# Performance work log

Hardware: AMD Instinct MI355X
Metric: run time of the kernel (lower is better)

## Reference

```python
import jax, jax.numpy as jnp
import numpy as np

BN_EPS = 1e-5
NN_EPS = 1e-8


def _three_nn_interp(xyz1, xyz2, points2):
    # xyz1: [B,N,3], xyz2: [B,S,3], points2: [B,S,D]
    # squared pairwise distances [B,N,S]
    d = (jnp.sum(xyz1 ** 2, -1)[:, :, None]
         + jnp.sum(xyz2 ** 2, -1)[:, None, :]
         - 2.0 * jnp.einsum('bnc,bsc->bns', xyz1, xyz2))
    neg_d3, idx = jax.lax.top_k(-d, 3)          # top-3 smallest dists
    d3 = -neg_d3                                # [B,N,3]
    recip = 1.0 / (d3 + NN_EPS)
    weight = recip / jnp.sum(recip, axis=2, keepdims=True)  # [B,N,3]
    gathered = jax.vmap(lambda p, i: p[i])(points2, idx)    # [B,N,3,D]
    return jnp.sum(gathered * weight[..., None], axis=2)    # [B,N,D]


def _conv_bn_relu(x, w, b, gamma, beta):
    # x: [B,C,N]; 1x1 conv == channel GEMM; BN in training mode (batch stats)
    y = jnp.einsum('oc,bcn->bon', w, x) + b[None, :, None]
    mean = jnp.mean(y, axis=(0, 2), keepdims=True)
    var = jnp.mean((y - mean) ** 2, axis=(0, 2), keepdims=True)
    y = (y - mean) * jax.lax.rsqrt(var + BN_EPS)
    y = y * gamma[None, :, None] + beta[None, :, None]
    return jax.nn.relu(y)


def setup_inputs() -> dict:
    key = jax.random.key(0)
    ks = jax.random.split(key, 8)
    B, N, S, D1, D2 = 8, 8192, 2048, 256, 256
    Cin, C0, C1 = D1 + D2, 256, 256
    return {
        'xyz1': jax.random.normal(ks[0], (B, 3, N), jnp.float32),
        'xyz2': jax.random.normal(ks[1], (B, 3, S), jnp.float32),
        'points1': jax.random.normal(ks[2], (B, D1, N), jnp.float32),
        'points2': jax.random.normal(ks[3], (B, D2, S), jnp.float32),
        'w0': jax.random.normal(ks[4], (C0, Cin), jnp.float32) * (1.0 / np.sqrt(Cin)),
        'b0': jnp.zeros((C0,), jnp.float32),
        'gamma0': jnp.ones((C0,), jnp.float32),
        'beta0': jnp.zeros((C0,), jnp.float32),
        'w1': jax.random.normal(ks[5], (C1, C0), jnp.float32) * (1.0 / np.sqrt(C0)),
        'b1': jnp.zeros((C1,), jnp.float32),
        'gamma1': jnp.ones((C1,), jnp.float32),
        'beta1': jnp.zeros((C1,), jnp.float32),
    }


def reference(xyz1, xyz2, points1, points2, w0, b0, gamma0, beta0, w1, b1, gamma1, beta1):
    x1 = jnp.transpose(xyz1, (0, 2, 1))     # [B,N,3]
    x2 = jnp.transpose(xyz2, (0, 2, 1))     # [B,S,3]
    p2 = jnp.transpose(points2, (0, 2, 1))  # [B,S,D2]
    interp = _three_nn_interp(x1, x2, p2)   # [B,N,D2]
    p1 = jnp.transpose(points1, (0, 2, 1))  # [B,N,D1]
    new_points = jnp.transpose(jnp.concatenate([p1, interp], axis=-1), (0, 2, 1))  # [B,Cin,N]
    h = _conv_bn_relu(new_points, w0, b0, gamma0, beta0)
    return _conv_bn_relu(h, w1, b1, gamma1, beta1)
```

## Files before the change

### kernel.cpp

```cpp
#include <hip/hip_runtime.h>
#include <math.h>

#define B 8
#define N 8192
#define S 2048
#define SCH 1024
#define C 256
#define CIN 512
#define CNT (B * N)
#define NSLOT 1024

typedef unsigned long long ull;
typedef __attribute__((ext_vector_type(8))) short bf16x8;
typedef __attribute__((ext_vector_type(4))) float floatx4;
typedef __attribute__((ext_vector_type(8))) unsigned short ushort8v;
typedef __attribute__((ext_vector_type(4))) unsigned short ushort4v;

__device__ inline unsigned short f2bf(float f) {
  unsigned u = __builtin_bit_cast(unsigned, f);
  u += 0x7FFF + ((u >> 16) & 1);
  return (unsigned short)(u >> 16);
}
__device__ inline float bf2f(unsigned short h) {
  unsigned u = ((unsigned)h) << 16;
  return __builtin_bit_cast(float, u);
}

__device__ inline void load_lds16(const void* g, void* l) {
  __builtin_amdgcn_global_load_lds(
      (const __attribute__((address_space(1))) unsigned int*)g,
      (__attribute__((address_space(3))) unsigned int*)l, 16, 0, 0);
}

__device__ inline void ins3u(ull k, ull& k0, ull& k1, ull& k2) {
  if (k < k2) {
    if (k < k1) {
      k2 = k1;
      if (k < k0) { k1 = k0; k0 = k; } else k1 = k;
    } else k2 = k;
  }
}

__device__ inline void insf(float k, float& m0, float& m1, float& m2) {
  float n1 = __builtin_amdgcn_fmed3f(k, m0, m1);
  float n2 = __builtin_amdgcn_fmed3f(k, m1, m2);
  m0 = fminf(k, m0);
  m1 = n1;
  m2 = n2;
}

__device__ inline unsigned sortkey(float f) {
  unsigned u = __float_as_uint(f);
  return u ^ (((unsigned)((int)u >> 31)) | 0x80000000u);
}
__device__ inline float unsortkey(unsigned u) {
  unsigned m = ((int)u < 0) ? 0x80000000u : 0xFFFFFFFFu;
  return __uint_as_float(u ^ m);
}

#define QDECL(q)                                                            \
  float d0_##q = INFINITY, d1_##q = INFINITY, d2_##q = INFINITY;            \
  float qx_##q, qy_##q, qz_##q, q2_##q;

#define QLOAD(q)                                                            \
  {                                                                         \
    float ox = p1[nq + q], oy = p1[N + nq + q], oz = p1[2 * N + nq + q];    \
    q2_##q = ox * ox + oy * oy + oz * oz;                                   \
    qx_##q = -2.0f * ox; qy_##q = -2.0f * oy; qz_##q = -2.0f * oz;          \
  }

#define QINSD(q)                                                            \
  {                                                                         \
    float d = fmaf(qx_##q, pc.x, fmaf(qy_##q, pc.y, fmaf(qz_##q, pc.z, pc.w))); \
    float n1 = __builtin_amdgcn_fmed3f(d, d0_##q, d1_##q);                  \
    float n2 = __builtin_amdgcn_fmed3f(d, d1_##q, d2_##q);                  \
    d0_##q = fminf(d, d0_##q);                                              \
    d1_##q = n1;                                                            \
    d2_##q = n2;                                                            \
  }

__global__ __launch_bounds__(256, 4) void nn3_kernel(const float* __restrict__ xyz1,
                                                     const float* __restrict__ xyz2,
                                                     const unsigned short* __restrict__ p2t,
                                                     unsigned short* __restrict__ Xb) {
  __shared__ float4 sp[SCH];
  __shared__ float t2q[32];
  __shared__ int ccnt[32];
  __shared__ float cand_d[32][8];
  __shared__ int cand_s[32][8];
  __shared__ int sidx[32][3];
  __shared__ float swt[32][3];
  int b = blockIdx.x >> 8;
  int n0 = (blockIdx.x & 255) * 32;
  const float* p2 = xyz2 + (size_t)b * 3 * S;
  int tid = threadIdx.x;
  int sub = tid & 15, grp = tid >> 4;
  const float* p1 = xyz1 + (size_t)b * 3 * N;
  int nq = n0 + grp * 2;
  QDECL(0) QDECL(1)
  QLOAD(0) QLOAD(1)

  for (int ch = 0; ch < 2; ++ch) {
    if (ch) __syncthreads();
    for (int i = tid; i < SCH; i += 256) {
      int g = ch * SCH + i;
      float px = p2[g], py = p2[S + g], pz = p2[2 * S + g];
      sp[i] = make_float4(px, py, pz, px * px + py * py + pz * pz);
    }
    __syncthreads();
    const float4* spp = sp + sub;
    float4 pc = spp[0];
    for (int t = 0; t < SCH / 16 - 1; ++t) {
      float4 pn = spp[(t + 1) * 16];
      QINSD(0) QINSD(1)
      pc = pn;
    }
    QINSD(0) QINSD(1)
  }

  __syncthreads();
  float* tm = (float*)sp;
  tm[((grp * 2 + 0) * 16 + sub) * 3 + 0] = d0_0;
  tm[((grp * 2 + 0) * 16 + sub) * 3 + 1] = d1_0;
  tm[((grp * 2 + 0) * 16 + sub) * 3 + 2] = d2_0;
  tm[((grp * 2 + 1) * 16 + sub) * 3 + 0] = d0_1;
  tm[((grp * 2 + 1) * 16 + sub) * 3 + 1] = d1_1;
  tm[((grp * 2 + 1) * 16 + sub) * 3 + 2] = d2_1;
  if (tid < 32) ccnt[tid] = 0;
  __syncthreads();
  if (sub < 4) {
#pragma unroll
    for (int q = 0; q < 2; ++q) {
      int qi = grp * 2 + q;
      float m0 = INFINITY, m1 = INFINITY, m2 = INFINITY;
#pragma unroll
      for (int jj = 0; jj < 4; ++jj) {
        int ss = sub + 4 * jj;
        insf(tm[(qi * 16 + ss) * 3 + 0], m0, m1, m2);
        insf(tm[(qi * 16 + ss) * 3 + 1], m0, m1, m2);
        insf(tm[(qi * 16 + ss) * 3 + 2], m0, m1, m2);
      }
#pragma unroll
      for (int mm = 1; mm <= 2; mm <<= 1) {
        float e0 = __shfl_xor(m0, mm);
        float e1 = __shfl_xor(m1, mm);
        float e2 = __shfl_xor(m2, mm);
        insf(e0, m0, m1, m2);
        insf(e1, m0, m1, m2);
        insf(e2, m0, m1, m2);
      }
      if (sub == 0) t2q[qi] = m2;
    }
  }
  __syncthreads();
  float t2_0 = t2q[grp * 2], t2_1 = t2q[grp * 2 + 1];

  for (int ch = 0; ch < 2; ++ch) {
    if (ch) __syncthreads();
    for (int i = tid; i < SCH; i += 256) {
      int g = ch * SCH + i;
      float px = p2[g], py = p2[S + g], pz = p2[2 * S + g];
      sp[i] = make_float4(px, py, pz, px * px + py * py + pz * pz);
    }
    __syncthreads();
    const float4* spp = sp + sub;
    for (int t = 0; t < SCH / 16; ++t) {
      float4 pc = spp[t * 16];
      int s = ch * SCH + t * 16 + sub;
      {
        float d = fmaf(qx_0, pc.x, fmaf(qy_0, pc.y, fmaf(qz_0, pc.z, pc.w)));
        if (d <= t2_0) {
          int sl = atomicAdd(&ccnt[grp * 2], 1);
          if (sl < 8) { cand_d[grp * 2][sl] = d; cand_s[grp * 2][sl] = s; }
        }
      }
      {
        float d = fmaf(qx_1, pc.x, fmaf(qy_1, pc.y, fmaf(qz_1, pc.z, pc.w)));
        if (d <= t2_1) {
          int sl = atomicAdd(&ccnt[grp * 2 + 1], 1);
          if (sl < 8) { cand_d[grp * 2 + 1][sl] = d; cand_s[grp * 2 + 1][sl] = s; }
        }
      }
    }
  }
  __syncthreads();

  if (sub == 0) {
#pragma unroll
    for (int q = 0; q < 2; ++q) {
      int qi = grp * 2 + q;
      int n = min(ccnt[qi], 8);
      ull k0 = ~0ull, k1 = ~0ull, k2 = ~0ull;
      for (int i = 0; i < n; ++i) {
        ull k = ((ull)sortkey(cand_d[qi][i]) << 32) | (unsigned)cand_s[qi][i];
        ins3u(k, k0, k1, k2);
      }
      float q2v = q ? q2_1 : q2_0;
      float e0 = fmaxf(unsortkey((unsigned)(k0 >> 32)) + q2v, 0.0f);
      float e1 = fmaxf(unsortkey((unsigned)(k1 >> 32)) + q2v, 0.0f);
      float e2 = fmaxf(unsortkey((unsigned)(k2 >> 32)) + q2v, 0.0f);
      float r0 = 1.0f / (e0 + 1e-8f);
      float r1 = 1.0f / (e1 + 1e-8f);
      float r2 = 1.0f / (e2 + 1e-8f);
      float rs = 1.0f / (r0 + r1 + r2);
      sidx[qi][0] = (int)(unsigned)k0;
      sidx[qi][1] = (int)(unsigned)k1;
      sidx[qi][2] = (int)(unsigned)k2;
      swt[qi][0] = r0 * rs;
      swt[qi][1] = r1 * rs;
      swt[qi][2] = r2 * rs;
    }
  }
  __syncthreads();

  int qi = tid >> 3, cc = tid & 7;
  int j0 = sidx[qi][0], j1 = sidx[qi][1], j2 = sidx[qi][2];
  float w0v = swt[qi][0], w1v = swt[qi][1], w2v = swt[qi][2];
  const unsigned short* pb = p2t + (size_t)b * S * 256;
  const unsigned short* r0p = pb + (size_t)j0 * 256;
  const unsigned short* r1p = pb + (size_t)j1 * 256;
  const unsigned short* r2p = pb + (size_t)j2 * 256;
  unsigned short* xp = Xb + ((size_t)b * N + n0 + qi) * 512 + 256;
#pragma unroll
  for (int h = 0; h < 4; ++h) {
    int co = (cc + h * 8) * 8;
    ushort8v v0 = *(const ushort8v*)(r0p + co);
    ushort8v v1 = *(const ushort8v*)(r1p + co);
    ushort8v v2 = *(const ushort8v*)(r2p + co);
    ushort8v o;
#pragma unroll
    for (int i = 0; i < 8; ++i)
      o[i] = f2bf(w0v * bf2f(v0[i]) + w1v * bf2f(v1[i]) + w2v * bf2f(v2[i]));
    *(ushort8v*)(xp + co) = o;
  }
}

__device__ inline void tconv_body(const float* __restrict__ src,
                                  unsigned short* __restrict__ dst,
                                  int cols, int drow, int bx, int by, int bz,
                                  float (*t)[65]) {
  int n0 = bx * 64, c0 = by * 64, b = bz;
  int tid = threadIdx.x, r = tid >> 2, q = tid & 3;
  const float* sp = src + ((size_t)b * 256 + c0 + r) * cols + n0 + q * 16;
#pragma unroll
  for (int i = 0; i < 4; ++i) {
    float4 v = *(const float4*)(sp + i * 4);
    t[r][q * 16 + i * 4 + 0] = v.x;
    t[r][q * 16 + i * 4 + 1] = v.y;
    t[r][q * 16 + i * 4 + 2] = v.z;
    t[r][q * 16 + i * 4 + 3] = v.w;
  }
  __syncthreads();
  unsigned short* dp = dst + ((size_t)b * cols + n0 + r) * drow + c0 + q * 16;
  ushort8v o0, o1;
#pragma unroll
  for (int i = 0; i < 8; ++i) o0[i] = f2bf(t[q * 16 + i][r]);
#pragma unroll
  for (int i = 0; i < 8; ++i) o1[i] = f2bf(t[q * 16 + 8 + i][r]);
  *(ushort8v*)dp = o0;
  *(ushort8v*)(dp + 8) = o1;
}

__global__ __launch_bounds__(256) void prep_kernel(const float* __restrict__ points1,
                                                   const float* __restrict__ points2,
                                                   const float* __restrict__ w0,
                                                   const float* __restrict__ w1,
                                                   unsigned short* __restrict__ Xb,
                                                   unsigned short* __restrict__ p2t,
                                                   unsigned short* __restrict__ w0b,
                                                   unsigned short* __restrict__ w1b) {
  __shared__ float t[64][65];
  int id = blockIdx.x;
  if (id < 4096) {
    tconv_body(points1, Xb, N, 512, id & 127, (id >> 7) & 3, id >> 9, t);
  } else if (id < 5120) {
    id -= 4096;
    tconv_body(points2, p2t, S, 256, id & 31, (id >> 5) & 3, id >> 7, t);
  } else {
    int i = (id - 5120) * 256 + threadIdx.x;
    if (i < C * CIN) w0b[i] = f2bf(w0[i]);
    else {
      int j = i - C * CIN;
      if (j < C * C) w1b[j] = f2bf(w1[j]);
    }
  }
}

__global__ __launch_bounds__(256) void gemm_kernel(const unsigned short* __restrict__ X,
                                                   const unsigned short* __restrict__ Wb,
                                                   const float* __restrict__ bias,
                                                   unsigned short* __restrict__ Y,
                                                   float* __restrict__ psum,
                                                   float* __restrict__ psumsq,
                                                   int Cin) {
  __shared__ unsigned short As[128 * 64];
  __shared__ unsigned short Bs[128 * 64];
  int n0 = blockIdx.x * 128, o0 = blockIdx.y * 128, b = blockIdx.z;
  int tid = threadIdx.x, lane = tid & 63, wid = tid >> 6;
  int wm = wid >> 1, wn = wid & 1;
  floatx4 acc[4][4];
#pragma unroll
  for (int m = 0; m < 4; ++m)
#pragma unroll
    for (int nt = 0; nt < 4; ++nt) acc[m][nt] = (floatx4)(0.0f);

  size_t rsA = (size_t)Cin * 2;
  int chunkSwz = ((lane & 7) ^ ((lane >> 3) & 7)) * 16;
  const char* Abase = (const char*)Wb + (size_t)(o0 + wid * 32 + (lane >> 3)) * rsA + chunkSwz;
  const char* Bbase = (const char*)X + ((size_t)b * N + n0 + wid * 32 + (lane >> 3)) * rsA + chunkSwz;
  size_t rstep8 = 8 * rsA;
  int fr = lane & 15;
  int cbase = lane >> 4;
  int rswz = lane & 7;

  for (int k0 = 0; k0 < Cin; k0 += 64) {
#pragma unroll
    for (int l = 0; l < 4; ++l) {
      load_lds16(Abase + (size_t)k0 * 2 + (size_t)l * rstep8, &As[(wid * 32 + l * 8) * 64]);
      load_lds16(Bbase + (size_t)k0 * 2 + (size_t)l * rstep8, &Bs[(wid * 32 + l * 8) * 64]);
    }
    __syncthreads();
#pragma unroll
    for (int kk = 0; kk < 2; ++kk) {
      int chunk = (cbase + kk * 4) ^ rswz;
      bf16x8 af[4], bfv[4];
#pragma unroll
      for (int m = 0; m < 4; ++m)
        af[m] = *(const bf16x8*)&As[(wm * 64 + m * 16 + fr) * 64 + chunk * 8];
#pragma unroll
      for (int nt = 0; nt < 4; ++nt)
        bfv[nt] = *(const bf16x8*)&Bs[(wn * 64 + nt * 16 + fr) * 64 + chunk * 8];
#pragma unroll
      for (int m = 0; m < 4; ++m)
#pragma unroll
        for (int nt = 0; nt < 4; ++nt)
          acc[m][nt] = __builtin_amdgcn_mfma_f32_16x16x32_bf16(af[m], bfv[nt], acc[m][nt], 0, 0, 0);
    }
    __syncthreads();
  }

  int col = lane & 15, rowq = lane >> 4;
  int slot = ((b * 64 + blockIdx.x) * 2) + wn;
#pragma unroll
  for (int m = 0; m < 4; ++m) {
    int ob = o0 + wm * 64 + m * 16 + rowq * 4;
    float4 bs = *(const float4*)&bias[ob];
    float sj[4] = {0.f, 0.f, 0.f, 0.f}, qj[4] = {0.f, 0.f, 0.f, 0.f};
#pragma unroll
    for (int nt = 0; nt < 4; ++nt) {
      int n = n0 + wn * 64 + nt * 16 + col;
      float y0 = acc[m][nt][0] + bs.x;
      float y1 = acc[m][nt][1] + bs.y;
      float y2 = acc[m][nt][2] + bs.z;
      float y3 = acc[m][nt][3] + bs.w;
      ushort4v v;
      v[0] = f2bf(y0); v[1] = f2bf(y1); v[2] = f2bf(y2); v[3] = f2bf(y3);
      *(ushort4v*)&Y[((size_t)b * N + n) * 256 + ob] = v;
      sj[0] += y0; qj[0] = fmaf(y0, y0, qj[0]);
      sj[1] += y1; qj[1] = fmaf(y1, y1, qj[1]);
      sj[2] += y2; qj[2] = fmaf(y2, y2, qj[2]);
      sj[3] += y3; qj[3] = fmaf(y3, y3, qj[3]);
    }
#pragma unroll
    for (int j = 0; j < 4; ++j) {
#pragma unroll
      for (int d = 1; d <= 8; d <<= 1) {
        sj[j] += __shfl_xor(sj[j], d);
        qj[j] += __shfl_xor(qj[j], d);
      }
    }
    if (col == 0) {
      int c0 = blockIdx.y * 128 + wm * 64 + m * 16 + rowq * 4;
#pragma unroll
      for (int j = 0; j < 4; ++j) {
        psum[(size_t)(c0 + j) * NSLOT + slot] = sj[j];
        psumsq[(size_t)(c0 + j) * NSLOT + slot] = qj[j];
      }
    }
  }
}

__global__ __launch_bounds__(256) void gemm_bn_kernel(const unsigned short* __restrict__ X,
                                                      const unsigned short* __restrict__ Wb,
                                                      const float* __restrict__ bias,
                                                      const float* __restrict__ scale,
                                                      const float* __restrict__ shift,
                                                      unsigned short* __restrict__ Y,
                                                      float* __restrict__ psum,
                                                      float* __restrict__ psumsq) {
  const int Cin = C;
  __shared__ unsigned short As[128 * 64];
  __shared__ unsigned short Bs[128 * 64];
  __shared__ float sscale[256], sshift[256];
  int n0 = blockIdx.x * 128, o0 = blockIdx.y * 128, b = blockIdx.z;
  int tid = threadIdx.x, lane = tid & 63, wid = tid >> 6;
  int wm = wid >> 1, wn = wid & 1;
  sscale[tid] = scale[tid];
  sshift[tid] = shift[tid];
  floatx4 acc[4][4];
#pragma unroll
  for (int m = 0; m < 4; ++m)
#pragma unroll
    for (int nt = 0; nt < 4; ++nt) acc[m][nt] = (floatx4)(0.0f);

  size_t rsA = (size_t)Cin * 2;
  int cg = (lane & 7) ^ ((lane >> 3) & 7);
  int chunkSwz = cg * 16;
  const char* Abase = (const char*)Wb + (size_t)(o0 + wid * 32 + (lane >> 3)) * rsA + chunkSwz;
  const char* Bbase = (const char*)X + ((size_t)b * N + n0 + wid * 32 + (lane >> 3)) * rsA + chunkSwz;
  size_t rstep8 = 8 * rsA;
  int fr = lane & 15;
  int cbase = lane >> 4;
  int rswz = lane & 7;
  __syncthreads();

  for (int k0 = 0; k0 < Cin; k0 += 64) {
    int kb = k0 + cg * 8;
    float4 sc0 = *(const float4*)&sscale[kb];
    float4 sc1 = *(const float4*)&sscale[kb + 4];
    float4 sh0 = *(const float4*)&sshift[kb];
    float4 sh1 = *(const float4*)&sshift[kb + 4];
#pragma unroll
    for (int l = 0; l < 4; ++l) {
      load_lds16(Abase + (size_t)k0 * 2 + (size_t)l * rstep8, &As[(wid * 32 + l * 8) * 64]);
      ushort8v raw = *(const ushort8v*)(Bbase + (size_t)k0 * 2 + (size_t)l * rstep8);
      ushort8v tv;
      tv[0] = f2bf(fmaxf(fmaf(bf2f(raw[0]), sc0.x, sh0.x), 0.f));
      tv[1] = f2bf(fmaxf(fmaf(bf2f(raw[1]), sc0.y, sh0.y), 0.f));
      tv[2] = f2bf(fmaxf(fmaf(bf2f(raw[2]), sc0.z, sh0.z), 0.f));
      tv[3] = f2bf(fmaxf(fmaf(bf2f(raw[3]), sc0.w, sh0.w), 0.f));
      tv[4] = f2bf(fmaxf(fmaf(bf2f(raw[4]), sc1.x, sh1.x), 0.f));
      tv[5] = f2bf(fmaxf(fmaf(bf2f(raw[5]), sc1.y, sh1.y), 0.f));
      tv[6] = f2bf(fmaxf(fmaf(bf2f(raw[6]), sc1.z, sh1.z), 0.f));
      tv[7] = f2bf(fmaxf(fmaf(bf2f(raw[7]), sc1.w, sh1.w), 0.f));
      *(ushort8v*)&Bs[(wid * 32 + l * 8) * 64 + lane * 8] = tv;
    }
    __syncthreads();
#pragma unroll
    for (int kk = 0; kk < 2; ++kk) {
      int chunk = (cbase + kk * 4) ^ rswz;
      bf16x8 af[4], bfv[4];
#pragma unroll
      for (int m = 0; m < 4; ++m)
        af[m] = *(const bf16x8*)&As[(wm * 64 + m * 16 + fr) * 64 + chunk * 8];
#pragma unroll
      for (int nt = 0; nt < 4; ++nt)
        bfv[nt] = *(const bf16x8*)&Bs[(wn * 64 + nt * 16 + fr) * 64 + chunk * 8];
#pragma unroll
      for (int m = 0; m < 4; ++m)
#pragma unroll
        for (int nt = 0; nt < 4; ++nt)
          acc[m][nt] = __builtin_amdgcn_mfma_f32_16x16x32_bf16(af[m], bfv[nt], acc[m][nt], 0, 0, 0);
    }
    __syncthreads();
  }

  int col = lane & 15, rowq = lane >> 4;
  int slot = ((b * 64 + blockIdx.x) * 2) + wn;
#pragma unroll
  for (int m = 0; m < 4; ++m) {
    int ob = o0 + wm * 64 + m * 16 + rowq * 4;
    float4 bs = *(const float4*)&bias[ob];
    float sj[4] = {0.f, 0.f, 0.f, 0.f}, qj[4] = {0.f, 0.f, 0.f, 0.f};
#pragma unroll
    for (int nt = 0; nt < 4; ++nt) {
      int n = n0 + wn * 64 + nt * 16 + col;
      float y0 = acc[m][nt][0] + bs.x;
      float y1 = acc[m][nt][1] + bs.y;
      float y2 = acc[m][nt][2] + bs.z;
      float y3 = acc[m][nt][3] + bs.w;
      ushort4v v;
      v[0] = f2bf(y0); v[1] = f2bf(y1); v[2] = f2bf(y2); v[3] = f2bf(y3);
      *(ushort4v*)&Y[((size_t)b * N + n) * 256 + ob] = v;
      sj[0] += y0; qj[0] = fmaf(y0, y0, qj[0]);
      sj[1] += y1; qj[1] = fmaf(y1, y1, qj[1]);
      sj[2] += y2; qj[2] = fmaf(y2, y2, qj[2]);
      sj[3] += y3; qj[3] = fmaf(y3, y3, qj[3]);
    }
#pragma unroll
    for (int j = 0; j < 4; ++j) {
#pragma unroll
      for (int d = 1; d <= 8; d <<= 1) {
        sj[j] += __shfl_xor(sj[j], d);
        qj[j] += __shfl_xor(qj[j], d);
      }
    }
    if (col == 0) {
      int c0 = blockIdx.y * 128 + wm * 64 + m * 16 + rowq * 4;
#pragma unroll
      for (int j = 0; j < 4; ++j) {
        psum[(size_t)(c0 + j) * NSLOT + slot] = sj[j];
        psumsq[(size_t)(c0 + j) * NSLOT + slot] = qj[j];
      }
    }
  }
}

__global__ __launch_bounds__(256) void bnparam_kernel(const float* __restrict__ psum,
                                                      const float* __restrict__ psumsq,
                                                      const float* __restrict__ gamma,
                                                      const float* __restrict__ beta,
                                                      float* __restrict__ scale,
                                                      float* __restrict__ shift) {
  int c = blockIdx.x, tid = threadIdx.x;
  const float* ps = psum + (size_t)c * NSLOT;
  const float* pq = psumsq + (size_t)c * NSLOT;
  float s = 0.f, q = 0.f;
#pragma unroll
  for (int i = 0; i < NSLOT / 256; ++i) {
    s += ps[tid + i * 256];
    q += pq[tid + i * 256];
  }
#pragma unroll
  for (int d = 1; d <= 32; d <<= 1) {
    s += __shfl_xor(s, d);
    q += __shfl_xor(q, d);
  }
  __shared__ float ls[4], lq[4];
  int wid = tid >> 6;
  if ((tid & 63) == 0) { ls[wid] = s; lq[wid] = q; }
  __syncthreads();
  if (tid == 0) {
    s = ls[0] + ls[1] + ls[2] + ls[3];
    q = lq[0] + lq[1] + lq[2] + lq[3];
    float m = s * (1.0f / CNT);
    float v = q * (1.0f / CNT) - m * m;
    float sc = gamma[c] * rsqrtf(v + 1e-5f);
    scale[c] = sc;
    shift[c] = beta[c] - m * sc;
  }
}

__global__ __launch_bounds__(256) void bnreluT_kernel(const unsigned short* __restrict__ Y,
                                                      const float* __restrict__ scale,
                                                      const float* __restrict__ shift,
                                                      float* __restrict__ out) {
  __shared__ float t[64][65];
  int n0 = blockIdx.x * 64, o0 = blockIdx.y * 64, b = blockIdx.z;
  int tid = threadIdx.x, r = tid >> 2, q = tid & 3;
  const unsigned short* yp = Y + ((size_t)b * N + n0 + r) * 256 + o0 + q * 16;
#pragma unroll
  for (int h = 0; h < 2; ++h) {
    ushort8v v = *(const ushort8v*)(yp + h * 8);
#pragma unroll
    for (int i = 0; i < 8; ++i) {
      int oc = q * 16 + h * 8 + i;
      float f = fmaxf(fmaf(bf2f(v[i]), scale[o0 + oc], shift[o0 + oc]), 0.f);
      t[oc][r] = f;
    }
  }
  __syncthreads();
  float* op = out + ((size_t)b * 256 + o0 + r) * N + n0 + q * 16;
#pragma unroll
  for (int i = 0; i < 4; ++i) {
    float4 v = make_float4(t[r][q * 16 + i * 4 + 0], t[r][q * 16 + i * 4 + 1],
                           t[r][q * 16 + i * 4 + 2], t[r][q * 16 + i * 4 + 3]);
    *(float4*)(op + i * 4) = v;
  }
}

extern "C" void kernel_launch(void* const* d_in, const int* in_sizes, int n_in,
                              void* d_out, int out_size, void* d_ws, size_t ws_size,
                              hipStream_t stream) {
  const float* xyz1 = (const float*)d_in[0];
  const float* xyz2 = (const float*)d_in[1];
  const float* points1 = (const float*)d_in[2];
  const float* points2 = (const float*)d_in[3];
  const float* w0 = (const float*)d_in[4];
  const float* b0 = (const float*)d_in[5];
  const float* g0 = (const float*)d_in[6];
  const float* be0 = (const float*)d_in[7];
  const float* w1 = (const float*)d_in[8];
  const float* b1 = (const float*)d_in[9];
  const float* g1 = (const float*)d_in[10];
  const float* be1 = (const float*)d_in[11];
  float* out = (float*)d_out;

  char* ws = (char*)d_ws;
  float* scale0 = (float*)ws;          ws += 256 * 4;
  float* shift0 = (float*)ws;          ws += 256 * 4;
  float* scale1 = (float*)ws;          ws += 256 * 4;
  float* shift1 = (float*)ws;          ws += 256 * 4;
  float* psum = (float*)ws;            ws += (size_t)C * NSLOT * 4;
  float* psumsq = (float*)ws;          ws += (size_t)C * NSLOT * 4;
  unsigned short* w0b = (unsigned short*)ws;  ws += (size_t)C * CIN * 2;
  unsigned short* w1b = (unsigned short*)ws;  ws += (size_t)C * C * 2;
  unsigned short* p2t = (unsigned short*)ws;  ws += (size_t)B * S * 256 * 2;
  unsigned short* Xb = (unsigned short*)ws;   ws += (size_t)B * N * 512 * 2;
  unsigned short* Yb = (unsigned short*)ws;   ws += (size_t)B * N * 256 * 2;
  unsigned short* Zb = Xb;

  prep_kernel<<<dim3(4096 + 1024 + 768), 256, 0, stream>>>(points1, points2, w0, w1,
                                                           Xb, p2t, w0b, w1b);
  nn3_kernel<<<dim3(B * N / 32), 256, 0, stream>>>(xyz1, xyz2, p2t, Xb);
  gemm_kernel<<<dim3(N / 128, 2, B), 256, 0, stream>>>(Xb, w0b, b0, Yb, psum, psumsq, CIN);
  bnparam_kernel<<<dim3(C), 256, 0, stream>>>(psum, psumsq, g0, be0, scale0, shift0);
  gemm_bn_kernel<<<dim3(N / 128, 2, B), 256, 0, stream>>>(Yb, w1b, b1, scale0, shift0,
                                                          Zb, psum, psumsq);
  bnparam_kernel<<<dim3(C), 256, 0, stream>>>(psum, psumsq, g1, be1, scale1, shift1);
  bnreluT_kernel<<<dim3(N / 64, 4, B), 256, 0, stream>>>(Zb, scale1, shift1, out);
}
```

Measured before the change: 187.4 us.

## Move points1 transpose into nn3 kernel to overlap with nearest-neighbor search

The points1 fp32-to-bf16 transpose into Xb moves out of the prep kernel and becomes extra blocks appended to the nn3 launch. The memory-bound transpose blocks can then run concurrently with the compute-bound 3-NN search blocks instead of serializing before them. The shared tile reused from the nn3 LDS buffer has no padding column, which introduces bank conflicts on the transposed reads.

```diff
diff --git a/kernel.cpp b/kernel.cpp
--- a/kernel.cpp
+++ b/kernel.cpp
@@ -82,6 +82,7 @@
 __global__ __launch_bounds__(256, 4) void nn3_kernel(const float* __restrict__ xyz1,
                                                      const float* __restrict__ xyz2,
                                                      const unsigned short* __restrict__ p2t,
+                                                     const float* __restrict__ points1,
                                                      unsigned short* __restrict__ Xb) {
   __shared__ float4 sp[SCH];
   __shared__ float t2q[32];
@@ -90,10 +91,38 @@
   __shared__ int cand_s[32][8];
   __shared__ int sidx[32][3];
   __shared__ float swt[32][3];
+  int tid = threadIdx.x;
+
+  if (blockIdx.x >= 2048) {
+    int id = blockIdx.x - 2048;
+    int bx = id & 127, by = (id >> 7) & 3, bz = id >> 9;
+    int n0 = bx * 64, c0 = by * 64;
+    float* t = (float*)sp;
+    int r = tid >> 2, q = tid & 3;
+    const float* srcp = points1 + ((size_t)bz * 256 + c0 + r) * N + n0 + q * 16;
+#pragma unroll
+    for (int i = 0; i < 4; ++i) {
+      float4 v = *(const float4*)(srcp + i * 4);
+      t[r * 64 + q * 16 + i * 4 + 0] = v.x;
+      t[r * 64 + q * 16 + i * 4 + 1] = v.y;
+      t[r * 64 + q * 16 + i * 4 + 2] = v.z;
+      t[r * 64 + q * 16 + i * 4 + 3] = v.w;
+    }
+    __syncthreads();
+    unsigned short* dp = Xb + ((size_t)bz * N + n0 + r) * 512 + c0 + q * 16;
+    ushort8v o0, o1;
+#pragma unroll
+    for (int i = 0; i < 8; ++i) o0[i] = f2bf(t[(q * 16 + i) * 64 + r]);
+#pragma unroll
+    for (int i = 0; i < 8; ++i) o1[i] = f2bf(t[(q * 16 + 8 + i) * 64 + r]);
+    *(ushort8v*)dp = o0;
+    *(ushort8v*)(dp + 8) = o1;
+    return;
+  }
+
   int b = blockIdx.x >> 8;
   int n0 = (blockIdx.x & 255) * 32;
   const float* p2 = xyz2 + (size_t)b * 3 * S;
-  int tid = threadIdx.x;
   int sub = tid & 15, grp = tid >> 4;
   const float* p1 = xyz1 + (size_t)b * 3 * N;
   int nq = n0 + grp * 2;
@@ -235,49 +264,38 @@
   }
 }
 
-__device__ inline void tconv_body(const float* __restrict__ src,
-                                  unsigned short* __restrict__ dst,
-                                  int cols, int drow, int bx, int by, int bz,
-                                  float (*t)[65]) {
-  int n0 = bx * 64, c0 = by * 64, b = bz;
-  int tid = threadIdx.x, r = tid >> 2, q = tid & 3;
-  const float* sp = src + ((size_t)b * 256 + c0 + r) * cols + n0 + q * 16;
-#pragma unroll
-  for (int i = 0; i < 4; ++i) {
-    float4 v = *(const float4*)(sp + i * 4);
-    t[r][q * 16 + i * 4 + 0] = v.x;
-    t[r][q * 16 + i * 4 + 1] = v.y;
-    t[r][q * 16 + i * 4 + 2] = v.z;
-    t[r][q * 16 + i * 4 + 3] = v.w;
-  }
-  __syncthreads();
-  unsigned short* dp = dst + ((size_t)b * cols + n0 + r) * drow + c0 + q * 16;
-  ushort8v o0, o1;
-#pragma unroll
-  for (int i = 0; i < 8; ++i) o0[i] = f2bf(t[q * 16 + i][r]);
-#pragma unroll
-  for (int i = 0; i < 8; ++i) o1[i] = f2bf(t[q * 16 + 8 + i][r]);
-  *(ushort8v*)dp = o0;
-  *(ushort8v*)(dp + 8) = o1;
-}
-
-__global__ __launch_bounds__(256) void prep_kernel(const float* __restrict__ points1,
-                                                   const float* __restrict__ points2,
+__global__ __launch_bounds__(256) void prep_kernel(const float* __restrict__ points2,
                                                    const float* __restrict__ w0,
                                                    const float* __restrict__ w1,
-                                                   unsigned short* __restrict__ Xb,
                                                    unsigned short* __restrict__ p2t,
                                                    unsigned short* __restrict__ w0b,
                                                    unsigned short* __restrict__ w1b) {
   __shared__ float t[64][65];
   int id = blockIdx.x;
-  if (id < 4096) {
-    tconv_body(points1, Xb, N, 512, id & 127, (id >> 7) & 3, id >> 9, t);
-  } else if (id < 5120) {
-    id -= 4096;
-    tconv_body(points2, p2t, S, 256, id & 31, (id >> 5) & 3, id >> 7, t);
+  if (id < 1024) {
+    int bx = id & 31, by = (id >> 5) & 3, bz = id >> 7;
+    int n0 = bx * 64, c0 = by * 64;
+    int tid = threadIdx.x, r = tid >> 2, q = tid & 3;
+    const float* sp = points2 + ((size_t)bz * 256 + c0 + r) * S + n0 + q * 16;
+#pragma unroll
+    for (int i = 0; i < 4; ++i) {
+      float4 v = *(const float4*)(sp + i * 4);
+      t[r][q * 16 + i * 4 + 0] = v.x;
+      t[r][q * 16 + i * 4 + 1] = v.y;
+      t[r][q * 16 + i * 4 + 2] = v.z;
+      t[r][q * 16 + i * 4 + 3] = v.w;
+    }
+    __syncthreads();
+    unsigned short* dp = p2t + ((size_t)bz * S + n0 + r) * 256 + c0 + q * 16;
+    ushort8v o0, o1;
+#pragma unroll
+    for (int i = 0; i < 8; ++i) o0[i] = f2bf(t[q * 16 + i][r]);
+#pragma unroll
+    for (int i = 0; i < 8; ++i) o1[i] = f2bf(t[q * 16 + 8 + i][r]);
+    *(ushort8v*)dp = o0;
+    *(ushort8v*)(dp + 8) = o1;
   } else {
-    int i = (id - 5120) * 256 + threadIdx.x;
+    int i = (id - 1024) * 256 + threadIdx.x;
     if (i < C * CIN) w0b[i] = f2bf(w0[i]);
     else {
       int j = i - C * CIN;
@@ -590,9 +608,8 @@
   unsigned short* Yb = (unsigned short*)ws;   ws += (size_t)B * N * 256 * 2;
   unsigned short* Zb = Xb;
 
-  prep_kernel<<<dim3(4096 + 1024 + 768), 256, 0, stream>>>(points1, points2, w0, w1,
-                                                           Xb, p2t, w0b, w1b);
-  nn3_kernel<<<dim3(B * N / 32), 256, 0, stream>>>(xyz1, xyz2, p2t, Xb);
+  prep_kernel<<<dim3(1024 + 768), 256, 0, stream>>>(points2, w0, w1, p2t, w0b, w1b);
+  nn3_kernel<<<dim3(2048 + 4096), 256, 0, stream>>>(xyz1, xyz2, p2t, points1, Xb);
   gemm_kernel<<<dim3(N / 128, 2, B), 256, 0, stream>>>(Xb, w0b, b0, Yb, psum, psumsq, CIN);
   bnparam_kernel<<<dim3(C), 256, 0, stream>>>(psum, psumsq, g0, be0, scale0, shift0);
   gemm_bn_kernel<<<dim3(N / 128, 2, B), 256, 0, stream>>>(Yb, w1b, b1, scale0, shift0,
```

Result: no change. 186.6 us (-0.4%).
